# Kernel optimization log

Hardware: AMD Instinct MI355X
Metric: run time of the kernel (lower is better)

Reference implementation:

```python
import jax, jax.numpy as jnp
import numpy as np

B, T, C, H = 2, 2048, 1024, 16
HD = C // H          # head dim = 64
HD2 = HD // 2        # rotary half = 32


def setup_inputs() -> dict:
    key = jax.random.key(0)
    k0, k1, k2 = jax.random.split(key, 3)
    x = jax.random.normal(k0, (B, T, C), jnp.float32)
    Wqkv = jax.random.normal(k1, (C, 3 * C), jnp.float32) * (1.0 / np.sqrt(C))
    bqkv = jnp.zeros((3 * C,), jnp.float32)
    Wproj = jax.random.normal(k2, (C, C), jnp.float32) * (1.0 / np.sqrt(C))
    bproj = jnp.zeros((C,), jnp.float32)
    # standard rotary frequencies: theta_i = 10000^{-2i/hd}
    inv_freq = 1.0 / (10000.0 ** (jnp.arange(0, HD, 2, dtype=jnp.float32) / HD))
    angles = jnp.arange(T, dtype=jnp.float32)[:, None] * inv_freq[None, :]  # (T, HD2)
    return {
        "x": x,
        "freqs_cos": jnp.cos(angles),
        "freqs_sin": jnp.sin(angles),
        "Wqkv": Wqkv,
        "bqkv": bqkv,
        "Wproj": Wproj,
        "bproj": bproj,
    }


def _rope(u, cos, sin):
    # u: (B, T, H, HD); half-split pairing: (u[i], u[i + HD/2]) form a complex pair
    u1, u2 = u[..., :HD2], u[..., HD2:]
    c = cos[None, :, None, :]  # (1, T, 1, HD2)
    s = sin[None, :, None, :]
    return jnp.concatenate([u1 * c - u2 * s, u1 * s + u2 * c], axis=-1)


def reference(x, freqs_cos, freqs_sin, Wqkv, bqkv, Wproj, bproj):
    Bc, Tc, Cc = x.shape
    qkv = x @ Wqkv + bqkv                      # (B, T, 3C)
    q, k, v = jnp.split(qkv, 3, axis=-1)
    q = q.reshape(Bc, Tc, H, HD)
    k = k.reshape(Bc, Tc, H, HD)
    v = v.reshape(Bc, Tc, H, HD)
    q = _rope(q, freqs_cos, freqs_sin)
    k = _rope(k, freqs_cos, freqs_sin)
    scale = 1.0 / np.sqrt(HD)
    scores = jnp.einsum("bthd,bshd->bhts", q, k) * scale  # (B, H, T, T)
    causal = jnp.tril(jnp.ones((Tc, Tc), dtype=bool))
    scores = jnp.where(causal[None, None], scores, jnp.finfo(scores.dtype).min)
    p = jax.nn.softmax(scores, axis=-1)
    y = jnp.einsum("bhts,bshd->bthd", p, v).reshape(Bc, Tc, Cc)
    return y @ Wproj + bproj
```

## Files before the change

kernel.cpp:

```cpp
#include <hip/hip_runtime.h>
#include <hip/hip_bf16.h>
#include <cstdint>
#include <cmath>

typedef __bf16 bf16_t;
typedef __attribute__((ext_vector_type(8))) __bf16 bf16x8;
typedef __attribute__((ext_vector_type(4))) float f32x4;

#define LOG2E 1.4426950408889634f

constexpr int B_ = 2, T_ = 2048, C_ = 1024, H_ = 16, HD_ = 64, HD2_ = 32;
constexpr int M_ = B_ * T_;

static __device__ __forceinline__ f32x4 mfma16(bf16x8 a, bf16x8 b, f32x4 c) {
    return __builtin_amdgcn_mfma_f32_16x16x32_bf16(a, b, c, 0, 0, 0);
}

#define GLL(gp, lp)                                                          \
    __builtin_amdgcn_global_load_lds(                                        \
        (const __attribute__((address_space(1))) void*)(gp),                 \
        (__attribute__((address_space(3))) void*)(lp), 16, 0, 0)

__global__ __launch_bounds__(256) void prep(
    const float* __restrict__ x, bf16_t* __restrict__ xb,
    const float* __restrict__ Wqkv, bf16_t* __restrict__ wqkvT,
    const float* __restrict__ Wproj, bf16_t* __restrict__ wprojT) {
    __shared__ float tile[32][33];
    const int bid = blockIdx.x, tid = threadIdx.x;
    if (bid < 512) {
#pragma unroll
        for (int it = 0; it < 8; it++) {
            int i = it * 131072 + bid * 256 + tid;
            float4 v = ((const float4*)x)[i];
            bf16_t o[4] = {(bf16_t)v.x, (bf16_t)v.y, (bf16_t)v.z, (bf16_t)v.w};
            *(uint64_t*)(xb + (size_t)i * 4) = *(uint64_t*)o;
        }
        return;
    }
    const float* W;
    bf16_t* WT;
    int N, base;
    bool qkv = (bid < 512 + 1536);
    if (qkv) {
        W = Wqkv; WT = wqkvT; N = 3 * C_;
        base = (bid - 512) * 2;
    } else {
        W = Wproj; WT = wprojT; N = C_;
        base = (bid - 2048) * 2;
    }
    const int tx = tid & 31, ty = tid >> 5;
    for (int u = 0; u < 2; u++) {
        int tt = base + u;
        int nb, kb;
        if (qkv) { nb = (tt % 96) * 32; kb = (tt / 96) * 32; }
        else     { nb = (tt & 31) * 32; kb = (tt >> 5) * 32; }
        __syncthreads();
        for (int i = ty; i < 32; i += 8)
            tile[i][tx] = W[(size_t)(kb + i) * N + nb + tx];
        __syncthreads();
        for (int i = ty; i < 32; i += 8)
            WT[(size_t)(nb + i) * C_ + kb + tx] = (bf16_t)tile[tx][i];
    }
}

template <int MODE>
__global__ __launch_bounds__(256, 3) void gemm128(
    const bf16_t* __restrict__ A, const bf16_t* __restrict__ BT, const float* __restrict__ bias,
    int N, int K,
    bf16_t* __restrict__ Qb, bf16_t* __restrict__ Kb, bf16_t* __restrict__ VTb,
    const float* __restrict__ cosT, const float* __restrict__ sinT, float* __restrict__ out) {
    constexpr int NT = (MODE == 1) ? 2 : 4;
    constexpr int BPARTS = (MODE == 1) ? 2 : 4;
    __shared__ alignas(16) bf16_t As[128 * 64];
    __shared__ alignas(16) bf16_t Bs[32 * BPARTS * 64];
    const int tid = threadIdx.x;
    const int w = tid >> 6, lane = tid & 63;
    const int quad = lane >> 4, r = lane & 15;
    const int wm = (w >> 1) * 64, wn = (w & 1) * (16 * NT);
    const int bid = blockIdx.x;
    const int xcd = bid & 7, s = bid >> 3;
    int mb, nb;
    if (MODE == 0) {
        mb = (((xcd >> 1) << 3) + (s & 7)) << 7;
        nb = (((xcd & 1) * 12 + (s >> 3))) << 7;
    } else {
        mb = (((xcd >> 1) << 3) + (s & 7)) << 7;
        nb = (((xcd & 1) << 3) + (s >> 3)) << 6;
    }
    const int srow = tid >> 3, schunk = tid & 7;
    const int csw = (schunk ^ (srow & 7)) * 8;
    const int koff0 = (quad ^ (r & 7)) * 8;
    const int koff1 = ((quad + 4) ^ (r & 7)) * 8;

    f32x4 acc[4][NT] = {};

    const bf16_t* gA[4];
    const bf16_t* gB[BPARTS];
#pragma unroll
    for (int p = 0; p < 4; p++) gA[p] = A + (size_t)(mb + p * 32 + srow) * K + csw;
#pragma unroll
    for (int p = 0; p < BPARTS; p++) gB[p] = BT + (size_t)(nb + p * 32 + srow) * K + csw;

    for (int k0 = 0; k0 < K; k0 += 64) {
        __syncthreads();
#pragma unroll
        for (int p = 0; p < 4; p++) GLL(gA[p] + k0, As + p * 2048 + tid * 8);
#pragma unroll
        for (int p = 0; p < BPARTS; p++) GLL(gB[p] + k0, Bs + p * 2048 + tid * 8);
        __syncthreads();
#pragma unroll
        for (int h = 0; h < 2; h++) {
            const int ko = h ? koff1 : koff0;
            bf16x8 af[4], bfr[NT];
#pragma unroll
            for (int i = 0; i < 4; i++) af[i] = *(const bf16x8*)(As + (wm + i * 16 + r) * 64 + ko);
#pragma unroll
            for (int j = 0; j < NT; j++) bfr[j] = *(const bf16x8*)(Bs + (wn + j * 16 + r) * 64 + ko);
#pragma unroll
            for (int i = 0; i < 4; i++)
#pragma unroll
                for (int j = 0; j < NT; j++) acc[i][j] = mfma16(af[i], bfr[j], acc[i][j]);
        }
    }

    if (MODE == 0) {
        const int col_base = nb + wn;
        const int region = col_base >> 10;
        const int h = (col_base & 1023) >> 6;
        const float qscale = 0.125f * LOG2E;
        if (region < 2) {
#pragma unroll
            for (int i = 0; i < 4; i++) {
#pragma unroll
                for (int g = 0; g < 4; g++) {
                    int m = mb + wm + i * 16 + quad * 4 + g;
                    int b = m >> 11, t = m & (T_ - 1);
                    bf16_t* dst = (region == 0 ? Qb : Kb) + ((size_t)((b * H_ + h) * T_ + t)) * 64;
                    int tw = t & 7;
#pragma unroll
                    for (int j = 0; j < 2; j++) {
                        int d = j * 16 + r;
                        float u1 = acc[i][j][g] + bias[col_base + d];
                        float u2 = acc[i][j + 2][g] + bias[col_base + d + 32];
                        float c = cosT[t * HD2_ + d], s2 = sinT[t * HD2_ + d];
                        float o1 = u1 * c - u2 * s2;
                        float o2 = u1 * s2 + u2 * c;
                        if (region == 0) {
                            dst[d] = (bf16_t)(o1 * qscale);
                            dst[d + 32] = (bf16_t)(o2 * qscale);
                        } else {
                            dst[((((d >> 3) ^ tw)) << 3) | (d & 7)] = (bf16_t)o1;
                            dst[(((((d + 32) >> 3) ^ tw)) << 3) | (d & 7)] = (bf16_t)o2;
                        }
                    }
                }
            }
        } else {
#pragma unroll
            for (int i = 0; i < 4; i++) {
                int m0 = mb + wm + i * 16 + quad * 4;
                int b = m0 >> 11, t0 = m0 & (T_ - 1);
                bf16_t* base = VTb + (size_t)(b * H_ + h) * 64 * T_;
#pragma unroll
                for (int j = 0; j < 4; j++) {
                    int d = j * 16 + r;
                    float bb = bias[col_base + d];
                    bf16_t pk[4];
#pragma unroll
                    for (int g = 0; g < 4; g++) pk[g] = (bf16_t)(acc[i][j][g] + bb);
                    int c = (((t0 >> 3) & 7) ^ (d & 7));
                    int tsw = (t0 & ~63) | (c << 3) | (t0 & 7);
                    *(uint64_t*)(base + (size_t)d * T_ + tsw) = *(uint64_t*)pk;
                }
            }
        }
    } else {
#pragma unroll
        for (int i = 0; i < 4; i++)
#pragma unroll
            for (int g = 0; g < 4; g++) {
                int m = mb + wm + i * 16 + quad * 4 + g;
#pragma unroll
                for (int j = 0; j < NT; j++) {
                    int col = nb + wn + j * 16 + r;
                    out[(size_t)m * N + col] = acc[i][j][g] + bias[col];
                }
            }
    }
}

__global__ __launch_bounds__(256, 2) void attn64(
    const bf16_t* __restrict__ Qb, const bf16_t* __restrict__ Kb,
    const bf16_t* __restrict__ VTb, bf16_t* __restrict__ att) {
    __shared__ alignas(16) bf16_t Ks[2][2][4096];
    __shared__ alignas(16) bf16_t Vs[2][2][4096];
    __shared__ alignas(16) bf16_t Ps[4][2048];
    const int tid = threadIdx.x;
    const int w = tid >> 6, lane = tid & 63;
    const int grp = w >> 1, wq = w & 1;
    const int quad = lane >> 4, r = lane & 15;
    const int id = blockIdx.x;
    const int t = 31 - (id >> 5);
    const int bh = id & 31;
    const int ntiles = t + 1, nstages = (t + 2) >> 1;
    const size_t kbase = (size_t)bh * T_ * 64;
    const size_t vbase = (size_t)bh * 64 * T_;
    bf16_t* Pw = &Ps[w][0];
    const int srow = tid >> 3, schunk = tid & 7;
    const int koff0 = ((quad ^ (r & 7)) * 8);
    const int koff1 = (((quad + 4) ^ (r & 7)) * 8);

    const int qbase = t * 64 + wq * 32;
    const int qrow0 = qbase + r, qrow1 = qbase + 16 + r;
    bf16x8 qf00 = *(const bf16x8*)(Qb + kbase + (size_t)qrow0 * 64 + quad * 8);
    bf16x8 qf01 = *(const bf16x8*)(Qb + kbase + (size_t)qrow0 * 64 + 32 + quad * 8);
    bf16x8 qf10 = *(const bf16x8*)(Qb + kbase + (size_t)qrow1 * 64 + quad * 8);
    bf16x8 qf11 = *(const bf16x8*)(Qb + kbase + (size_t)qrow1 * 64 + 32 + quad * 8);

    f32x4 oacc[4][2] = {};
    float l0 = 0.f, l1 = 0.f;

    {
        const bf16_t* kg = Kb + kbase + (size_t)srow * 64 + schunk * 8;
        const bf16_t* vg = VTb + vbase + (size_t)srow * T_ + schunk * 8;
        GLL(kg, &Ks[0][0][0] + tid * 8);
        GLL(kg + 2048, &Ks[0][0][0] + 2048 + tid * 8);
        GLL(vg, &Vs[0][0][0] + tid * 8);
        GLL(vg + 32 * T_, &Vs[0][0][0] + 2048 + tid * 8);
        if (1 < ntiles) {
            GLL(kg + 4096, &Ks[0][1][0] + tid * 8);
            GLL(kg + 4096 + 2048, &Ks[0][1][0] + 2048 + tid * 8);
            GLL(vg + 64, &Vs[0][1][0] + tid * 8);
            GLL(vg + 32 * T_ + 64, &Vs[0][1][0] + 2048 + tid * 8);
        }
    }
    for (int s = 0; s < nstages; s++) {
        const int cur = s & 1;
        __syncthreads();
        if (s + 1 < nstages) {
            const int ja = 2 * (s + 1);
            const bf16_t* kg = Kb + kbase + (size_t)(ja * 64 + srow) * 64 + schunk * 8;
            const bf16_t* vg = VTb + vbase + (size_t)srow * T_ + ja * 64 + schunk * 8;
            GLL(kg, &Ks[cur ^ 1][0][0] + tid * 8);
            GLL(kg + 2048, &Ks[cur ^ 1][0][0] + 2048 + tid * 8);
            GLL(vg, &Vs[cur ^ 1][0][0] + tid * 8);
            GLL(vg + 32 * T_, &Vs[cur ^ 1][0][0] + 2048 + tid * 8);
            if (ja + 1 < ntiles) {
                GLL(kg + 4096, &Ks[cur ^ 1][1][0] + tid * 8);
                GLL(kg + 4096 + 2048, &Ks[cur ^ 1][1][0] + 2048 + tid * 8);
                GLL(vg + 64, &Vs[cur ^ 1][1][0] + tid * 8);
                GLL(vg + 32 * T_ + 64, &Vs[cur ^ 1][1][0] + 2048 + tid * 8);
            }
        }
        const int jt = 2 * s + grp;
        if (jt < ntiles) {
            const bf16_t* Kt = &Ks[cur][grp][0];
            const bf16_t* Vt = &Vs[cur][grp][0];
            f32x4 sc[4][2];
            __builtin_amdgcn_s_setprio(1);
#pragma unroll
            for (int m0 = 0; m0 < 4; m0++) {
                const bf16_t* kp = Kt + (m0 * 16 + r) * 64;
                bf16x8 kf0 = *(const bf16x8*)(kp + koff0);
                bf16x8 kf1 = *(const bf16x8*)(kp + koff1);
                f32x4 z0 = {0.f, 0.f, 0.f, 0.f};
                z0 = mfma16(kf0, qf00, z0);
                z0 = mfma16(kf1, qf01, z0);
                sc[m0][0] = z0;
                f32x4 z1 = {0.f, 0.f, 0.f, 0.f};
                z1 = mfma16(kf0, qf10, z1);
                z1 = mfma16(kf1, qf11, z1);
                sc[m0][1] = z1;
            }
            __builtin_amdgcn_s_setprio(0);
            if (jt == t) {
                const int j0 = jt * 64;
#pragma unroll
                for (int m0 = 0; m0 < 4; m0++) {
                    int kvb = j0 + m0 * 16 + quad * 4;
#pragma unroll
                    for (int g = 0; g < 4; g++) {
                        if (kvb + g > qrow0) sc[m0][0][g] = -INFINITY;
                        if (kvb + g > qrow1) sc[m0][1][g] = -INFINITY;
                    }
                }
            }
            float rs0 = 0.f, rs1 = 0.f;
#pragma unroll
            for (int m0 = 0; m0 < 4; m0++)
#pragma unroll
                for (int g = 0; g < 4; g++) {
                    float p0 = __builtin_amdgcn_exp2f(sc[m0][0][g]);
                    float p1 = __builtin_amdgcn_exp2f(sc[m0][1][g]);
                    sc[m0][0][g] = p0;
                    sc[m0][1][g] = p1;
                    rs0 += p0;
                    rs1 += p1;
                }
            l0 += rs0;
            l1 += rs1;
#pragma unroll
            for (int jq = 0; jq < 2; jq++)
#pragma unroll
                for (int m0 = 0; m0 < 4; m0++) {
                    bf16_t hq[4];
#pragma unroll
                    for (int g = 0; g < 4; g++) hq[g] = (bf16_t)sc[m0][jq][g];
                    int elem = jq * 1024 + (m0 >> 1) * 512 +
                               (((m0 & 1) * 2 + (quad >> 1)) * 16 + r) * 8 + (quad & 1) * 4;
                    *(uint64_t*)(Pw + elem) = *(uint64_t*)hq;
                }
            __builtin_amdgcn_wave_barrier();
            bf16x8 pf00 = *(const bf16x8*)(Pw + lane * 8);
            bf16x8 pf01 = *(const bf16x8*)(Pw + 512 + lane * 8);
            bf16x8 pf10 = *(const bf16x8*)(Pw + 1024 + lane * 8);
            bf16x8 pf11 = *(const bf16x8*)(Pw + 1536 + lane * 8);
            __builtin_amdgcn_s_setprio(1);
#pragma unroll
            for (int d0 = 0; d0 < 4; d0++) {
                const bf16_t* vp = Vt + (d0 * 16 + r) * 64;
                bf16x8 vf0 = *(const bf16x8*)(vp + koff0);
                bf16x8 vf1 = *(const bf16x8*)(vp + koff1);
                oacc[d0][0] = mfma16(vf0, pf00, oacc[d0][0]);
                oacc[d0][0] = mfma16(vf1, pf01, oacc[d0][0]);
                oacc[d0][1] = mfma16(vf0, pf10, oacc[d0][1]);
                oacc[d0][1] = mfma16(vf1, pf11, oacc[d0][1]);
            }
            __builtin_amdgcn_s_setprio(0);
        }
    }
    l0 += __shfl_xor(l0, 16);
    l0 += __shfl_xor(l0, 32);
    l1 += __shfl_xor(l1, 16);
    l1 += __shfl_xor(l1, 32);
    __syncthreads();
    float* Co = (float*)&Ks[0][0][0];
    float* Cl = (float*)&Vs[0][0][0];
    if (grp == 1) {
#pragma unroll
        for (int jq = 0; jq < 2; jq++)
#pragma unroll
            for (int d0 = 0; d0 < 4; d0++)
                *(f32x4*)(Co + ((wq * 2 + jq) * 16 + r) * 64 + d0 * 16 + quad * 4) =
                    oacc[d0][jq];
        if (quad == 0) {
            Cl[(wq * 2) * 16 + r] = l0;
            Cl[(wq * 2 + 1) * 16 + r] = l1;
        }
    }
    __syncthreads();
    if (grp == 0) {
        const int b = bh >> 4, h = bh & 15;
#pragma unroll
        for (int jq = 0; jq < 2; jq++) {
            float lsum = (jq ? l1 : l0) + Cl[(wq * 2 + jq) * 16 + r];
            float inv = 1.f / lsum;
            const int qrow = qbase + jq * 16 + r;
            bf16_t* dst = att + ((size_t)(b * T_ + qrow)) * 1024 + h * 64;
#pragma unroll
            for (int d0 = 0; d0 < 4; d0++) {
                f32x4 o1 =
                    *(const f32x4*)(Co + ((wq * 2 + jq) * 16 + r) * 64 + d0 * 16 + quad * 4);
                bf16_t hh[4];
#pragma unroll
                for (int g = 0; g < 4; g++)
                    hh[g] = (bf16_t)((oacc[d0][jq][g] + o1[g]) * inv);
                *(uint64_t*)(dst + d0 * 16 + quad * 4) = *(uint64_t*)hh;
            }
        }
    }
}

extern "C" void kernel_launch(void* const* d_in, const int* in_sizes, int n_in,
                              void* d_out, int out_size, void* d_ws, size_t ws_size,
                              hipStream_t stream) {
    const float* x = (const float*)d_in[0];
    const float* fcos = (const float*)d_in[1];
    const float* fsin = (const float*)d_in[2];
    const float* Wqkv = (const float*)d_in[3];
    const float* bqkv = (const float*)d_in[4];
    const float* Wproj = (const float*)d_in[5];
    const float* bproj = (const float*)d_in[6];
    float* out = (float*)d_out;

    uint8_t* p = (uint8_t*)d_ws;
    size_t need = 0;
    auto take = [&](size_t bytes) {
        void* q = p;
        size_t pad = (bytes + 255) & ~(size_t)255;
        p += pad;
        need += pad;
        return q;
    };
    bf16_t* xb = (bf16_t*)take((size_t)M_ * C_ * 2);
    bf16_t* wqkvT = (bf16_t*)take((size_t)3 * C_ * C_ * 2);
    bf16_t* wprojT = (bf16_t*)take((size_t)C_ * C_ * 2);
    bf16_t* Qb = (bf16_t*)take((size_t)B_ * H_ * T_ * 64 * 2);
    bf16_t* Kb = (bf16_t*)take((size_t)B_ * H_ * T_ * 64 * 2);
    bf16_t* VTb = (bf16_t*)take((size_t)B_ * H_ * 64 * T_ * 2);
    bf16_t* attb = (bf16_t*)take((size_t)M_ * C_ * 2);
    if (ws_size < need) return;

    prep<<<2560, 256, 0, stream>>>(x, xb, Wqkv, wqkvT, Wproj, wprojT);

    gemm128<0><<<dim3(768), 256, 0, stream>>>(
        xb, wqkvT, bqkv, 3 * C_, C_, Qb, Kb, VTb, fcos, fsin, nullptr);

    attn64<<<dim3(1024), 256, 0, stream>>>(Qb, Kb, VTb, attb);

    gemm128<1><<<dim3(512), 256, 0, stream>>>(
        attb, wprojT, bproj, C_, C_, nullptr, nullptr, nullptr, nullptr, nullptr, out);
}
```

Measured before the change: 171.5 us.

## Double-buffer GEMM LDS tiles and add explicit load drains before barriers

The GEMM main loop now keeps two LDS buffers and issues global-to-LDS loads for the next K-slice while MFMAs run on the current one, so load latency overlaps with compute. For the QKV GEMM the occupancy hint drops from 3 to 2 blocks per CU to make room for the doubled shared memory. Explicit s_waitcnt drains are placed before barriers in both the GEMM and the attention kernel so that asynchronous LDS loads have landed before any wave reads them. This is a correctness safeguard that may add stalls, and the lower occupancy could reduce latency hiding across blocks.

```diff
diff --git a/kernel.cpp b/kernel.cpp
--- a/kernel.cpp
+++ b/kernel.cpp
@@ -20,6 +20,8 @@
     __builtin_amdgcn_global_load_lds(                                        \
         (const __attribute__((address_space(1))) void*)(gp),                 \
         (__attribute__((address_space(3))) void*)(lp), 16, 0, 0)
+
+#define GLL_DRAIN() asm volatile("s_waitcnt vmcnt(0) lgkmcnt(0)" ::: "memory")
 
 __global__ __launch_bounds__(256) void prep(
     const float* __restrict__ x, bf16_t* __restrict__ xb,
@@ -64,15 +66,15 @@
 }
 
 template <int MODE>
-__global__ __launch_bounds__(256, 3) void gemm128(
+__global__ __launch_bounds__(256, (MODE == 1) ? 3 : 2) void gemm128(
     const bf16_t* __restrict__ A, const bf16_t* __restrict__ BT, const float* __restrict__ bias,
     int N, int K,
     bf16_t* __restrict__ Qb, bf16_t* __restrict__ Kb, bf16_t* __restrict__ VTb,
     const float* __restrict__ cosT, const float* __restrict__ sinT, float* __restrict__ out) {
     constexpr int NT = (MODE == 1) ? 2 : 4;
     constexpr int BPARTS = (MODE == 1) ? 2 : 4;
-    __shared__ alignas(16) bf16_t As[128 * 64];
-    __shared__ alignas(16) bf16_t Bs[32 * BPARTS * 64];
+    __shared__ alignas(16) bf16_t As[2][128 * 64];
+    __shared__ alignas(16) bf16_t Bs[2][32 * BPARTS * 64];
     const int tid = threadIdx.x;
     const int w = tid >> 6, lane = tid & 63;
     const int quad = lane >> 4, r = lane & 15;
@@ -101,26 +103,40 @@
 #pragma unroll
     for (int p = 0; p < BPARTS; p++) gB[p] = BT + (size_t)(nb + p * 32 + srow) * K + csw;
 
-    for (int k0 = 0; k0 < K; k0 += 64) {
-        __syncthreads();
-#pragma unroll
-        for (int p = 0; p < 4; p++) GLL(gA[p] + k0, As + p * 2048 + tid * 8);
-#pragma unroll
-        for (int p = 0; p < BPARTS; p++) GLL(gB[p] + k0, Bs + p * 2048 + tid * 8);
-        __syncthreads();
+    auto stage = [&](int b, int k) {
+#pragma unroll
+        for (int p = 0; p < 4; p++) GLL(gA[p] + k, &As[b][0] + p * 2048 + tid * 8);
+#pragma unroll
+        for (int p = 0; p < BPARTS; p++) GLL(gB[p] + k, &Bs[b][0] + p * 2048 + tid * 8);
+    };
+    auto compute = [&](int b) {
 #pragma unroll
         for (int h = 0; h < 2; h++) {
             const int ko = h ? koff1 : koff0;
             bf16x8 af[4], bfr[NT];
 #pragma unroll
-            for (int i = 0; i < 4; i++) af[i] = *(const bf16x8*)(As + (wm + i * 16 + r) * 64 + ko);
-#pragma unroll
-            for (int j = 0; j < NT; j++) bfr[j] = *(const bf16x8*)(Bs + (wn + j * 16 + r) * 64 + ko);
-#pragma unroll
             for (int i = 0; i < 4; i++)
+                af[i] = *(const bf16x8*)(&As[b][0] + (wm + i * 16 + r) * 64 + ko);
+#pragma unroll
+            for (int j = 0; j < NT; j++)
+                bfr[j] = *(const bf16x8*)(&Bs[b][0] + (wn + j * 16 + r) * 64 + ko);
+#pragma unroll
+            for (int i = 0; i < 4; i++)
 #pragma unroll
                 for (int j = 0; j < NT; j++) acc[i][j] = mfma16(af[i], bfr[j], acc[i][j]);
         }
+    };
+
+    stage(0, 0);
+    for (int k0 = 0; k0 < K; k0 += 128) {
+        GLL_DRAIN();
+        __syncthreads();
+        if (k0 + 64 < K) stage(1, k0 + 64);
+        compute(0);
+        GLL_DRAIN();
+        __syncthreads();
+        if (k0 + 128 < K) stage(0, k0 + 128);
+        compute(1);
     }
 
     if (MODE == 0) {
@@ -236,6 +252,7 @@
     }
     for (int s = 0; s < nstages; s++) {
         const int cur = s & 1;
+        GLL_DRAIN();
         __syncthreads();
         if (s + 1 < nstages) {
             const int ja = 2 * (s + 1);
@@ -333,6 +350,7 @@
     l0 += __shfl_xor(l0, 32);
     l1 += __shfl_xor(l1, 16);
     l1 += __shfl_xor(l1, 32);
+    GLL_DRAIN();
     __syncthreads();
     float* Co = (float*)&Ks[0][0][0];
     float* Cl = (float*)&Vs[0][0][0];
```

Result: slower. 183.3 us (+6.8%).
